# Optimization experiments

Hardware: AMD Instinct MI355X
Metric: run time of the kernel (lower is better)

The kernel has to match this reference:

```python
import jax, jax.numpy as jnp
import numpy as np

N_NODES = 50000
NUM_FEATURES = 64
HIDDEN = 512
NUM_CLASSES = 2
N_EDGES = 800000
BN_EPS = 1e-5


def setup_inputs() -> dict:
    key = jax.random.key(0)
    ks = jax.random.split(key, 10)
    x = jax.random.normal(ks[0], (N_NODES, NUM_FEATURES), dtype=jnp.float32)
    edge_index = jax.random.randint(ks[1], (2, N_EDGES), 0, N_NODES, dtype=jnp.int64)
    # GINConv MLP: Linear(F,H) -> ReLU -> Linear(H,H)
    W1 = jax.random.normal(ks[2], (NUM_FEATURES, HIDDEN), dtype=jnp.float32) * 0.05
    b1 = jnp.zeros((HIDDEN,), dtype=jnp.float32)
    W2 = jax.random.normal(ks[3], (HIDDEN, HIDDEN), dtype=jnp.float32) * 0.05
    b2 = jnp.zeros((HIDDEN,), dtype=jnp.float32)
    # BatchNorm1d(HIDDEN) affine params
    gamma = jnp.ones((HIDDEN,), dtype=jnp.float32)
    beta = jnp.zeros((HIDDEN,), dtype=jnp.float32)
    # classifier: Linear(HIDDEN, NUM_CLASSES)
    Wc = jax.random.normal(ks[4], (HIDDEN, NUM_CLASSES), dtype=jnp.float32) * 0.05
    bc = jnp.zeros((NUM_CLASSES,), dtype=jnp.float32)
    return {"x": x, "edge_index": edge_index, "W1": W1, "b1": b1,
            "W2": W2, "b2": b2, "gamma": gamma, "beta": beta,
            "Wc": Wc, "bc": bc}


def reference(x, edge_index, W1, b1, W2, b2, gamma, beta, Wc, bc):
    # NOTE: the original torch forward returns inside the loop, so exactly ONE
    # GINConv layer runs, followed by batchnorm, relu, dropout(p=0), classifier.
    src, dst = edge_index[0], edge_index[1]
    # GINConv (eps=0): h_i = MLP(x_i + sum_{j -> i} x_j)
    agg = jax.ops.segment_sum(x[src], dst, num_segments=x.shape[0])  # [N, F]
    h = x + agg
    h = jax.nn.relu(h @ W1 + b1) @ W2 + b2  # [N, H]
    # BatchNorm1d in training mode: normalize with batch statistics (biased var)
    mean = jnp.mean(h, axis=0)
    var = jnp.var(h, axis=0)
    h = (h - mean) * jax.lax.rsqrt(var + BN_EPS) * gamma + beta
    h = jax.nn.relu(h)
    # dropout p=0.0 is a no-op
    return h @ Wc + bc  # [N, NUM_CLASSES]
```

## Files before the change

### kernel.cpp

```cpp
#include <hip/hip_runtime.h>
#include <hip/hip_bf16.h>

#define NN 50000
#define MP 50176
#define NF 64
#define NH 512
#define NE 800000
#define NBK 196
#define EBCAP 8192
#define ABLK 391
#define MB 392
#define GRID (MB * 4)
#define CPX (GRID / 8)

typedef __attribute__((ext_vector_type(8))) short bf16x8;
typedef __attribute__((ext_vector_type(4))) float f32x4;

#define GLOAD16(g, l)                                                        \
    __builtin_amdgcn_global_load_lds(                                        \
        (const __attribute__((address_space(1))) unsigned int*)(g),          \
        (__attribute__((address_space(3))) unsigned int*)(l), 16, 0, 0)

__device__ __forceinline__ float bfu(unsigned short u) {
    union { float f; unsigned int i; } c;
    c.i = ((unsigned int)u) << 16;
    return c.f;
}

__global__ void detect_idx(const int* __restrict__ ei, int* __restrict__ flag) {
    if (threadIdx.x == 0 && blockIdx.x == 0) {
        int any = 0;
        for (int i = 0; i < 32; ++i) any |= ei[2 * i + 1];
        *flag = (any == 0) ? 1 : 0;
    }
}

__global__ __launch_bounds__(256) void bucketA(const void* __restrict__ eiv,
                                               const int* __restrict__ flag,
                                               int* __restrict__ bcnt,
                                               int* __restrict__ ebP) {
    __shared__ int hist[NBK];
    __shared__ int lcur[NBK];
    const int tid = threadIdx.x;
    const int chunk = blockIdx.x * 2048;
    const int lim = min(2048, NE - chunk);
    const bool is64 = (*flag != 0);
    const long long* ei64 = (const long long*)eiv;
    const int* ei32 = (const int*)eiv;

    for (int i = tid; i < NBK; i += 256) hist[i] = 0;
    __syncthreads();
    for (int i = tid; i < lim; i += 256) {
        int d = is64 ? (int)ei64[NE + chunk + i] : ei32[NE + chunk + i];
        atomicAdd(&hist[d >> 8], 1);
    }
    __syncthreads();
    for (int i = tid; i < NBK; i += 256) {
        int c = hist[i];
        lcur[i] = c ? atomicAdd(&bcnt[i], c) : 0;
    }
    __syncthreads();
    for (int i = tid; i < lim; i += 256) {
        int s, d;
        if (is64) { s = (int)ei64[chunk + i]; d = (int)ei64[NE + chunk + i]; }
        else      { s = ei32[chunk + i];      d = ei32[NE + chunk + i]; }
        int b = d >> 8;
        int p = atomicAdd(&lcur[b], 1);
        ebP[b * EBCAP + p] = ((d & 255) << 16) | s;
    }
}

__global__ __launch_bounds__(256) void scan_bsum(const int* __restrict__ bsum,
                                                 int* __restrict__ boff) {
    __shared__ int sm[256];
    int tid = threadIdx.x;
    int v = (tid < NBK) ? bsum[tid] : 0;
    sm[tid] = v;
    __syncthreads();
    int acc = v;
#pragma unroll
    for (int off = 1; off < 256; off <<= 1) {
        int t = (tid >= off) ? sm[tid - off] : 0;
        __syncthreads();
        acc += t;
        sm[tid] = acc;
        __syncthreads();
    }
    if (tid < NBK) boff[tid] = acc - v;
}

__global__ __launch_bounds__(256) void bucketB(const int* __restrict__ ebP,
                                               const int* __restrict__ bcnt,
                                               const int* __restrict__ bbase,
                                               int* __restrict__ rowptr,
                                               int* __restrict__ csr) {
    __shared__ int hist[256], sm[256], curs[256];
    const int b = blockIdx.x;
    const int tid = threadIdx.x;
    const int n0 = b << 8;
    const int cnt = bcnt[b];
    const int base = bbase[b];

    hist[tid] = 0;
    __syncthreads();
    for (int i = tid; i < cnt; i += 256)
        atomicAdd(&hist[(ebP[b * EBCAP + i] >> 16) & 255], 1);
    __syncthreads();
    int v = hist[tid];
    sm[tid] = v;
    __syncthreads();
    int acc = v;
#pragma unroll
    for (int off = 1; off < 256; off <<= 1) {
        int t = (tid >= off) ? sm[tid - off] : 0;
        __syncthreads();
        acc += t;
        sm[tid] = acc;
        __syncthreads();
    }
    int excl = acc - v;
    if (n0 + tid < NN) rowptr[n0 + tid] = base + excl;
    curs[tid] = excl;
    __syncthreads();
    for (int i = tid; i < cnt; i += 256) {
        int p = ebP[b * EBCAP + i];
        int lp = atomicAdd(&curs[(p >> 16) & 255], 1);
        csr[base + lp] = p & 0xFFFF;
    }
    if (b == 0 && tid == 0) rowptr[NN] = NE;
}

#define XBLK  (NN * NF / 4 / 256)
#define W1BLK (NF * NH / 256)
#define W2BLK (NH * NH / 256)
__global__ __launch_bounds__(256) void cvt_all(const float* __restrict__ x,
                                               const float* __restrict__ W1,
                                               const float* __restrict__ W2,
                                               __hip_bfloat16* __restrict__ xb,
                                               __hip_bfloat16* __restrict__ w1t,
                                               __hip_bfloat16* __restrict__ w2t) {
    int bb = blockIdx.x;
    if (bb < XBLK) {
        int t = bb * 256 + threadIdx.x;
        float4 v = *(const float4*)&x[t * 4];
        union { ushort4 u; __hip_bfloat16 h[4]; } o;
        o.h[0] = __float2bfloat16(v.x);
        o.h[1] = __float2bfloat16(v.y);
        o.h[2] = __float2bfloat16(v.z);
        o.h[3] = __float2bfloat16(v.w);
        *(ushort4*)&xb[t * 4] = o.u;
    } else if (bb < XBLK + W1BLK) {
        int t = (bb - XBLK) * 256 + threadIdx.x;
        int n = t % NH, k = t / NH;
        w1t[n * NF + k] = __float2bfloat16(W1[t]);
    } else {
        int t = (bb - XBLK - W1BLK) * 256 + threadIdx.x;
        int n = t % NH, k = t / NH;
        w2t[n * NH + k] = __float2bfloat16(W2[t]);
    }
}

__global__ __launch_bounds__(256) void gather(const __hip_bfloat16* __restrict__ xb,
                                              const int* __restrict__ rowptr,
                                              const int* __restrict__ csr,
                                              __hip_bfloat16* __restrict__ h0b) {
    int n = blockIdx.x * 4 + (threadIdx.x >> 6);
    int lane = threadIdx.x & 63;
    int g = lane >> 4;
    int f4 = (lane & 15) * 4;
    if (n >= MP) return;
    if (n >= NN) {
        if (g == 0)
            *(ushort4*)&h0b[(long long)n * NF + f4] = make_ushort4(0, 0, 0, 0);
        return;
    }
    float a0 = 0.f, a1 = 0.f, a2 = 0.f, a3 = 0.f;
    if (g == 0) {
        ushort4 v = *(const ushort4*)&xb[(long long)n * NF + f4];
        a0 = bfu(v.x); a1 = bfu(v.y); a2 = bfu(v.z); a3 = bfu(v.w);
    }
    int e0 = rowptr[n], e1 = rowptr[n + 1];
    for (int e = e0 + g; e < e1; e += 4) {
        int s = csr[e];
        ushort4 v = *(const ushort4*)&xb[(long long)s * NF + f4];
        a0 += bfu(v.x); a1 += bfu(v.y); a2 += bfu(v.z); a3 += bfu(v.w);
    }
    a0 += __shfl_xor(a0, 16); a0 += __shfl_xor(a0, 32);
    a1 += __shfl_xor(a1, 16); a1 += __shfl_xor(a1, 32);
    a2 += __shfl_xor(a2, 16); a2 += __shfl_xor(a2, 32);
    a3 += __shfl_xor(a3, 16); a3 += __shfl_xor(a3, 32);
    if (g == 0) {
        union { ushort4 u; __hip_bfloat16 h[4]; } o;
        o.h[0] = __float2bfloat16(a0);
        o.h[1] = __float2bfloat16(a1);
        o.h[2] = __float2bfloat16(a2);
        o.h[3] = __float2bfloat16(a3);
        *(ushort4*)&h0b[(long long)n * NF + f4] = o.u;
    }
}

__global__ __launch_bounds__(256) void gemm1_staged(const __hip_bfloat16* __restrict__ A,
                                                    const __hip_bfloat16* __restrict__ BT,
                                                    const float* __restrict__ bias,
                                                    __hip_bfloat16* __restrict__ C) {
    __shared__ __hip_bfloat16 As[128 * 64];
    const int orig = blockIdx.x;
    const int L = (orig & 7) * CPX + (orig >> 3);
    const int mb = L >> 2, nb = L & 3;

    const int tid = threadIdx.x;
    const int lane = tid & 63;
    const int w = tid >> 6;
    const int wm = w >> 1, wn = w & 1;
    const long long rbase = (long long)mb * 128;
    const int nbase = nb * 128;
    const int r8  = lane >> 3;
    const int swc = (lane & 7) ^ r8;
    const int key = lane & 7;
    const int lo = lane & 15, hi = lane >> 4;

    {
        const __hip_bfloat16* ga = A + (rbase + w * 32 + r8) * NF + swc * 8;
        __hip_bfloat16* la = As + (w * 32) * 64;
#pragma unroll
        for (int t = 0; t < 4; ++t)
            GLOAD16(ga + t * 8 * NF, la + t * 8 * 64);
    }
    bf16x8 bfr[2][4];
#pragma unroll
    for (int ks = 0; ks < 2; ++ks)
#pragma unroll
        for (int ni = 0; ni < 4; ++ni)
            bfr[ks][ni] = *(const bf16x8*)&BT[(nbase + wn * 64 + ni * 16 + lo) * NF +
                                             ks * 32 + hi * 8];
    __syncthreads();

    f32x4 acc[4][4];
#pragma unroll
    for (int i = 0; i < 4; ++i)
#pragma unroll
        for (int j = 0; j < 4; ++j) acc[i][j] = (f32x4){0.f, 0.f, 0.f, 0.f};

#pragma unroll
    for (int ks = 0; ks < 2; ++ks) {
        bf16x8 af[4];
#pragma unroll
        for (int mi = 0; mi < 4; ++mi)
            af[mi] = *(const bf16x8*)&As[(wm * 64 + mi * 16 + lo) * 64 +
                                         (((ks * 4 + hi) ^ key) * 8)];
#pragma unroll
        for (int mi = 0; mi < 4; ++mi)
#pragma unroll
            for (int ni = 0; ni < 4; ++ni)
                acc[mi][ni] = __builtin_amdgcn_mfma_f32_16x16x32_bf16(
                    af[mi], bfr[ks][ni], acc[mi][ni], 0, 0, 0);
    }

    const int col0 = nbase + wn * 64 + lo;
    const long long row00 = rbase + wm * 64 + hi * 4;
#pragma unroll
    for (int ni = 0; ni < 4; ++ni) {
        int col = col0 + ni * 16;
        float bv = bias[col];
#pragma unroll
        for (int mi = 0; mi < 4; ++mi) {
            long long r0 = row00 + mi * 16;
#pragma unroll
            for (int r = 0; r < 4; ++r) {
                float v = fmaxf(acc[mi][ni][r] + bv, 0.f);
                C[(r0 + r) * NH + col] = __float2bfloat16(v);
            }
        }
    }
}

__global__ __launch_bounds__(256) void gemm2_db(const __hip_bfloat16* __restrict__ A,
                                                const __hip_bfloat16* __restrict__ BT,
                                                const float* __restrict__ bias,
                                                __hip_bfloat16* __restrict__ C,
                                                float* __restrict__ partial) {
    constexpr int BK = 64;
    __shared__ __align__(16) char smem[65536];
    float* smsum = (float*)smem;
    float* smsq  = (float*)(smem + 2048);

    const int orig = blockIdx.x;
    const int L = (orig & 7) * CPX + (orig >> 3);
    const int mb = L >> 2, nb = L & 3;

    const int tid = threadIdx.x;
    const int lane = tid & 63;
    const int w = tid >> 6;
    const int wm = w >> 1, wn = w & 1;
    const long long rbase = (long long)mb * 128;
    const int nbase = nb * 128;
    const int r8  = lane >> 3;
    const int swc = (lane & 7) ^ r8;
    const int key = lane & 7;
    const int lo = lane & 15, hi = lane >> 4;

    const __hip_bfloat16* gaBase =
        A + (rbase + w * 32 + r8) * (long long)NH + swc * 8;
    const __hip_bfloat16* gbBase =
        BT + (long long)(nbase + w * 32 + r8) * NH + swc * 8;
    const int laOff = (w * 32) * BK;

    auto STAGE = [&](int s, int kb) {
        __hip_bfloat16* la = (__hip_bfloat16*)(smem + s * 32768) + laOff;
        __hip_bfloat16* lb = (__hip_bfloat16*)(smem + s * 32768 + 16384) + laOff;
#pragma unroll
        for (int t = 0; t < 4; ++t)
            GLOAD16(gaBase + kb + (long long)t * 8 * NH, la + t * 8 * BK);
#pragma unroll
        for (int t = 0; t < 4; ++t)
            GLOAD16(gbBase + kb + (long long)t * 8 * NH, lb + t * 8 * BK);
    };

    f32x4 acc[4][4];
#pragma unroll
    for (int i = 0; i < 4; ++i)
#pragma unroll
        for (int j = 0; j < 4; ++j) acc[i][j] = (f32x4){0.f, 0.f, 0.f, 0.f};

    STAGE(0, 0);
    STAGE(1, BK);

#pragma unroll
    for (int t = 0; t < 8; ++t) {
        if (t == 7) { asm volatile("s_waitcnt vmcnt(0)" ::: "memory"); }
        else        { asm volatile("s_waitcnt vmcnt(8)" ::: "memory"); }
        __builtin_amdgcn_s_barrier();
        __builtin_amdgcn_sched_barrier(0);

        const __hip_bfloat16* Ac = (const __hip_bfloat16*)(smem + (t & 1) * 32768);
        const __hip_bfloat16* Bc = Ac + 8192;
        __builtin_amdgcn_s_setprio(1);
#pragma unroll
        for (int ks = 0; ks < 2; ++ks) {
            bf16x8 af[4], bfr[4];
#pragma unroll
            for (int mi = 0; mi < 4; ++mi)
                af[mi] = *(const bf16x8*)&Ac[(wm * 64 + mi * 16 + lo) * BK +
                                             (((ks * 4 + hi) ^ key) * 8)];
#pragma unroll
            for (int ni = 0; ni < 4; ++ni)
                bfr[ni] = *(const bf16x8*)&Bc[(wn * 64 + ni * 16 + lo) * BK +
                                              (((ks * 4 + hi) ^ key) * 8)];
#pragma unroll
            for (int mi = 0; mi < 4; ++mi)
#pragma unroll
                for (int ni = 0; ni < 4; ++ni)
                    acc[mi][ni] = __builtin_amdgcn_mfma_f32_16x16x32_bf16(
                        af[mi], bfr[ni], acc[mi][ni], 0, 0, 0);
        }
        __builtin_amdgcn_s_setprio(0);
        __builtin_amdgcn_sched_barrier(0);
        __builtin_amdgcn_s_barrier();
        __builtin_amdgcn_sched_barrier(0);
        if (t < 6) STAGE(t & 1, (t + 2) * BK);
    }

    __syncthreads();
    if (tid < 128) { smsum[tid] = 0.f; smsq[tid] = 0.f; }
    __syncthreads();
    const int col0 = nbase + wn * 64 + lo;
    const long long row00 = rbase + wm * 64 + hi * 4;
#pragma unroll
    for (int ni = 0; ni < 4; ++ni) {
        int col = col0 + ni * 16;
        float bv = bias[col];
        float s = 0.f, q = 0.f;
#pragma unroll
        for (int mi = 0; mi < 4; ++mi) {
            long long r0 = row00 + mi * 16;
#pragma unroll
            for (int r = 0; r < 4; ++r) {
                float v = acc[mi][ni][r] + bv;
                C[(r0 + r) * NH + col] = __float2bfloat16(v);
                if ((r0 + r) < NN) { s += v; q += v * v; }
            }
        }
        s += __shfl_xor(s, 16); s += __shfl_xor(s, 32);
        q += __shfl_xor(q, 16); q += __shfl_xor(q, 32);
        if (lane < 16) {
            atomicAdd(&smsum[wn * 64 + ni * 16 + lane], s);
            atomicAdd(&smsq[wn * 64 + ni * 16 + lane], q);
        }
    }
    __syncthreads();
    if (tid < 128) {
        partial[mb * 1024 + nbase + tid] = smsum[tid];
        partial[mb * 1024 + 512 + nbase + tid] = smsq[tid];
    }
}

__global__ __launch_bounds__(256) void stats_reduce(const float* __restrict__ partial,
                                                    float* __restrict__ stats) {
    int j = blockIdx.x * 256 + threadIdx.x;
    float s = 0.f;
    for (int mb = 0; mb < MB; ++mb) s += partial[mb * 1024 + j];
    stats[j] = s;
}

__global__ __launch_bounds__(256) void bn_cls(const __hip_bfloat16* __restrict__ h2b,
                                              const float* __restrict__ stats,
                                              const float* __restrict__ gamma,
                                              const float* __restrict__ beta,
                                              const float* __restrict__ Wc,
                                              const float* __restrict__ bc,
                                              float* __restrict__ out) {
    int tid = threadIdx.x;
    int lane = tid & 63;
    int k0 = lane * 8;
    float sc[8], sh[8], w0[8], w1[8];
#pragma unroll
    for (int j = 0; j < 8; ++j) {
        int k = k0 + j;
        float mean = stats[k] * (1.0f / NN);
        float var = stats[512 + k] * (1.0f / NN) - mean * mean;
        float rs = rsqrtf(var + 1e-5f);
        float s = gamma[k] * rs;
        sc[j] = s;
        sh[j] = beta[k] - mean * s;
        w0[j] = Wc[2 * k];
        w1[j] = Wc[2 * k + 1];
    }
    float bc0 = bc[0], bc1 = bc[1];
    int wid = blockIdx.x * 4 + (tid >> 6);
    int nw = gridDim.x * 4;
    for (int row = wid; row < NN; row += nw) {
        bf16x8 v8 = *(const bf16x8*)&h2b[(long long)row * NH + k0];
        float a0 = 0.f, a1 = 0.f;
#pragma unroll
        for (int j = 0; j < 8; ++j) {
            float v = __bfloat162float(((const __hip_bfloat16*)&v8)[j]);
            float hn = fmaxf(fmaf(v, sc[j], sh[j]), 0.f);
            a0 = fmaf(hn, w0[j], a0);
            a1 = fmaf(hn, w1[j], a1);
        }
#pragma unroll
        for (int off = 32; off; off >>= 1) {
            a0 += __shfl_xor(a0, off);
            a1 += __shfl_xor(a1, off);
        }
        if (lane == 0) {
            out[(long long)row * 2 + 0] = a0 + bc0;
            out[(long long)row * 2 + 1] = a1 + bc1;
        }
    }
}

extern "C" void kernel_launch(void* const* d_in, const int* in_sizes, int n_in,
                              void* d_out, int out_size, void* d_ws, size_t ws_size,
                              hipStream_t stream) {
    const float* x     = (const float*)d_in[0];
    const void*  ei    = d_in[1];
    const float* W1    = (const float*)d_in[2];
    const float* b1    = (const float*)d_in[3];
    const float* W2    = (const float*)d_in[4];
    const float* b2    = (const float*)d_in[5];
    const float* gamma = (const float*)d_in[6];
    const float* beta  = (const float*)d_in[7];
    const float* Wc    = (const float*)d_in[8];
    const float* bc    = (const float*)d_in[9];
    float* out = (float*)d_out;

    char* base = (char*)d_ws;
    size_t o = 0;
    auto alloc = [&](size_t bytes) {
        char* p = base + o;
        o = (o + bytes + 255) & ~(size_t)255;
        return p;
    };
    __hip_bfloat16* h0b     = (__hip_bfloat16*)alloc((size_t)MP * NF * 2);
    __hip_bfloat16* h1b     = (__hip_bfloat16*)alloc((size_t)MP * NH * 2);
    __hip_bfloat16* h2b     = (__hip_bfloat16*)alloc((size_t)MP * NH * 2);
    __hip_bfloat16* xb      = (__hip_bfloat16*)alloc((size_t)NN * NF * 2);
    __hip_bfloat16* w1t     = (__hip_bfloat16*)alloc((size_t)NH * NF * 2);
    __hip_bfloat16* w2t     = (__hip_bfloat16*)alloc((size_t)NH * NH * 2);
    int*            ebP     = (int*)alloc((size_t)NBK * EBCAP * 4);
    int*            bcnt    = (int*)alloc(256 * 4);
    int*            bbase   = (int*)alloc(256 * 4);
    int*            rowptr  = (int*)alloc((size_t)(NN + 1) * 4);
    int*            csr     = (int*)alloc((size_t)NE * 4);
    float*          partial = (float*)alloc((size_t)MB * 1024 * 4);
    float*          stats   = (float*)alloc(1024 * 4);
    int*            flag    = (int*)alloc(256);

    hipMemsetAsync(bcnt, 0, NBK * 4, stream);
    detect_idx<<<1, 1, 0, stream>>>((const int*)ei, flag);

    bucketA<<<ABLK, 256, 0, stream>>>(ei, flag, bcnt, ebP);
    scan_bsum<<<1, 256, 0, stream>>>(bcnt, bbase);
    bucketB<<<NBK, 256, 0, stream>>>(ebP, bcnt, bbase, rowptr, csr);

    cvt_all<<<XBLK + W1BLK + W2BLK, 256, 0, stream>>>(x, W1, W2, xb, w1t, w2t);
    gather<<<MP / 4, 256, 0, stream>>>(xb, rowptr, csr, h0b);

    gemm1_staged<<<GRID, 256, 0, stream>>>(h0b, w1t, b1, h1b);
    gemm2_db<<<GRID, 256, 0, stream>>>(h1b, w2t, b2, h2b, partial);

    stats_reduce<<<4, 256, 0, stream>>>(partial, stats);
    bn_cls<<<512, 256, 0, stream>>>(h2b, stats, gamma, beta, Wc, bc, out);
}
```

Baseline: 165.9 us.

## Keep full weight panel resident in LDS and loop blocks over M-tiles in gemm2

Replaces the 128x128-tile second GEMM with a persistent-style kernel. Each 512-thread block loads an entire 128-column by 512-deep W2 panel into LDS once, then streams seven 128-row A tiles through a double buffer. This aims to stop re-fetching B for every output tile and to cut the block count. BN partial statistics are now written per warp-row without an LDS atomic reduction, which doubles the partial buffer and the stats_reduce loop length. The 160KB LDS footprint allows only one block per CU, and 224 blocks leave some CUs idle.

```diff
diff --git a/kernel.cpp b/kernel.cpp
--- a/kernel.cpp
+++ b/kernel.cpp
@@ -12,6 +12,9 @@
 #define MB 392
 #define GRID (MB * 4)
 #define CPX (GRID / 8)
+#define G2BLK 224
+#define CPX2 (G2BLK / 8)
+#define MTPB 7
 
 typedef __attribute__((ext_vector_type(8))) short bf16x8;
 typedef __attribute__((ext_vector_type(4))) float f32x4;
@@ -274,123 +277,128 @@
     }
 }
 
-__global__ __launch_bounds__(256) void gemm2_db(const __hip_bfloat16* __restrict__ A,
-                                                const __hip_bfloat16* __restrict__ BT,
-                                                const float* __restrict__ bias,
-                                                __hip_bfloat16* __restrict__ C,
-                                                float* __restrict__ partial) {
+__global__ __launch_bounds__(512) void gemm2_panel(const __hip_bfloat16* __restrict__ A,
+                                                   const __hip_bfloat16* __restrict__ BT,
+                                                   const float* __restrict__ bias,
+                                                   __hip_bfloat16* __restrict__ C,
+                                                   float* __restrict__ partial) {
     constexpr int BK = 64;
-    __shared__ __align__(16) char smem[65536];
-    float* smsum = (float*)smem;
-    float* smsq  = (float*)(smem + 2048);
+    __shared__ __align__(16) char smem[163840];
+    __hip_bfloat16* Bp = (__hip_bfloat16*)smem;
+    __hip_bfloat16* Ab0 = (__hip_bfloat16*)(smem + 131072);
+    __hip_bfloat16* Ab1 = (__hip_bfloat16*)(smem + 147456);
 
     const int orig = blockIdx.x;
-    const int L = (orig & 7) * CPX + (orig >> 3);
-    const int mb = L >> 2, nb = L & 3;
+    const int L = (orig & 7) * CPX2 + (orig >> 3);
+    const int stripe = L / 56;
+    const int q = L % 56;
+    const int nbase = stripe * 128;
 
     const int tid = threadIdx.x;
     const int lane = tid & 63;
     const int w = tid >> 6;
-    const int wm = w >> 1, wn = w & 1;
-    const long long rbase = (long long)mb * 128;
-    const int nbase = nb * 128;
-    const int r8  = lane >> 3;
+    const int wm = w >> 2, wn = w & 3;
+    const int r8 = lane >> 3;
     const int swc = (lane & 7) ^ r8;
-    const int key = lane & 7;
     const int lo = lane & 15, hi = lane >> 4;
 
-    const __hip_bfloat16* gaBase =
-        A + (rbase + w * 32 + r8) * (long long)NH + swc * 8;
-    const __hip_bfloat16* gbBase =
-        BT + (long long)(nbase + w * 32 + r8) * NH + swc * 8;
-    const int laOff = (w * 32) * BK;
-
-    auto STAGE = [&](int s, int kb) {
-        __hip_bfloat16* la = (__hip_bfloat16*)(smem + s * 32768) + laOff;
-        __hip_bfloat16* lb = (__hip_bfloat16*)(smem + s * 32768 + 16384) + laOff;
-#pragma unroll
-        for (int t = 0; t < 4; ++t)
-            GLOAD16(gaBase + kb + (long long)t * 8 * NH, la + t * 8 * BK);
-#pragma unroll
-        for (int t = 0; t < 4; ++t)
-            GLOAD16(gbBase + kb + (long long)t * 8 * NH, lb + t * 8 * BK);
-    };
-
-    f32x4 acc[4][4];
-#pragma unroll
-    for (int i = 0; i < 4; ++i)
-#pragma unroll
-        for (int j = 0; j < 4; ++j) acc[i][j] = (f32x4){0.f, 0.f, 0.f, 0.f};
-
-    STAGE(0, 0);
-    STAGE(1, BK);
-
-#pragma unroll
-    for (int t = 0; t < 8; ++t) {
-        if (t == 7) { asm volatile("s_waitcnt vmcnt(0)" ::: "memory"); }
-        else        { asm volatile("s_waitcnt vmcnt(8)" ::: "memory"); }
-        __builtin_amdgcn_s_barrier();
-        __builtin_amdgcn_sched_barrier(0);
-
-        const __hip_bfloat16* Ac = (const __hip_bfloat16*)(smem + (t & 1) * 32768);
-        const __hip_bfloat16* Bc = Ac + 8192;
-        __builtin_amdgcn_s_setprio(1);
-#pragma unroll
-        for (int ks = 0; ks < 2; ++ks) {
-            bf16x8 af[4], bfr[4];
-#pragma unroll
-            for (int mi = 0; mi < 4; ++mi)
-                af[mi] = *(const bf16x8*)&Ac[(wm * 64 + mi * 16 + lo) * BK +
-                                             (((ks * 4 + hi) ^ key) * 8)];
-#pragma unroll
-            for (int ni = 0; ni < 4; ++ni)
-                bfr[ni] = *(const bf16x8*)&Bc[(wn * 64 + ni * 16 + lo) * BK +
-                                              (((ks * 4 + hi) ^ key) * 8)];
-#pragma unroll
-            for (int mi = 0; mi < 4; ++mi)
-#pragma unroll
-                for (int ni = 0; ni < 4; ++ni)
-                    acc[mi][ni] = __builtin_amdgcn_mfma_f32_16x16x32_bf16(
-                        af[mi], bfr[ni], acc[mi][ni], 0, 0, 0);
-        }
-        __builtin_amdgcn_s_setprio(0);
-        __builtin_amdgcn_sched_barrier(0);
-        __builtin_amdgcn_s_barrier();
-        __builtin_amdgcn_sched_barrier(0);
-        if (t < 6) STAGE(t & 1, (t + 2) * BK);
-    }
-
-    __syncthreads();
-    if (tid < 128) { smsum[tid] = 0.f; smsq[tid] = 0.f; }
-    __syncthreads();
-    const int col0 = nbase + wn * 64 + lo;
-    const long long row00 = rbase + wm * 64 + hi * 4;
-#pragma unroll
-    for (int ni = 0; ni < 4; ++ni) {
-        int col = col0 + ni * 16;
-        float bv = bias[col];
-        float s = 0.f, q = 0.f;
-#pragma unroll
-        for (int mi = 0; mi < 4; ++mi) {
-            long long r0 = row00 + mi * 16;
-#pragma unroll
-            for (int r = 0; r < 4; ++r) {
-                float v = acc[mi][ni][r] + bv;
-                C[(r0 + r) * NH + col] = __float2bfloat16(v);
-                if ((r0 + r) < NN) { s += v; q += v * v; }
+    {
+        const int colbase = w * 16;
+#pragma unroll
+        for (int c = 0; c < 16; ++c) {
+            int col = colbase + c;
+            int gch = (lane & ~7) | ((lane & 7) ^ (col & 7));
+            GLOAD16(BT + (long long)(nbase + col) * NH + gch * 8,
+                    Bp + col * 512 + lane * 8);
+        }
+    }
+    __syncthreads();
+
+    for (int mt = 0; mt < MTPB; ++mt) {
+        const int mb = q * MTPB + mt;
+        const long long rbase = (long long)mb * 128;
+        const __hip_bfloat16* gaBase =
+            A + (rbase + w * 16 + r8) * (long long)NH + swc * 8;
+        __hip_bfloat16* laBase0 = Ab0 + (w * 16) * BK;
+        __hip_bfloat16* laBase1 = Ab1 + (w * 16) * BK;
+
+        auto STAGE = [&](int s, int kb) {
+            __hip_bfloat16* la = s ? laBase1 : laBase0;
+#pragma unroll
+            for (int t = 0; t < 2; ++t)
+                GLOAD16(gaBase + kb + (long long)t * 8 * NH, la + t * 8 * BK);
+        };
+
+        f32x4 acc[4][2];
+#pragma unroll
+        for (int i = 0; i < 4; ++i)
+#pragma unroll
+            for (int j = 0; j < 2; ++j) acc[i][j] = (f32x4){0.f, 0.f, 0.f, 0.f};
+
+        STAGE(0, 0);
+        STAGE(1, BK);
+
+#pragma unroll
+        for (int t = 0; t < 8; ++t) {
+            if (t == 7) { asm volatile("s_waitcnt vmcnt(0)" ::: "memory"); }
+            else        { asm volatile("s_waitcnt vmcnt(2)" ::: "memory"); }
+            __builtin_amdgcn_s_barrier();
+            __builtin_amdgcn_sched_barrier(0);
+
+            const __hip_bfloat16* Ac = (t & 1) ? Ab1 : Ab0;
+#pragma unroll
+            for (int ks = 0; ks < 2; ++ks) {
+                bf16x8 af[4], bfr[2];
+#pragma unroll
+                for (int mi = 0; mi < 4; ++mi) {
+                    int row = wm * 64 + mi * 16 + lo;
+                    af[mi] = *(const bf16x8*)&Ac[row * BK +
+                                                 (((ks * 4 + hi) ^ (row & 7)) * 8)];
+                }
+#pragma unroll
+                for (int ni = 0; ni < 2; ++ni) {
+                    int col = wn * 32 + ni * 16 + lo;
+                    bfr[ni] = *(const bf16x8*)&Bp[col * 512 + t * 64 +
+                                                  (((ks * 4 + hi) ^ (col & 7)) * 8)];
+                }
+#pragma unroll
+                for (int mi = 0; mi < 4; ++mi)
+#pragma unroll
+                    for (int ni = 0; ni < 2; ++ni)
+                        acc[mi][ni] = __builtin_amdgcn_mfma_f32_16x16x32_bf16(
+                            af[mi], bfr[ni], acc[mi][ni], 0, 0, 0);
             }
-        }
-        s += __shfl_xor(s, 16); s += __shfl_xor(s, 32);
-        q += __shfl_xor(q, 16); q += __shfl_xor(q, 32);
-        if (lane < 16) {
-            atomicAdd(&smsum[wn * 64 + ni * 16 + lane], s);
-            atomicAdd(&smsq[wn * 64 + ni * 16 + lane], q);
-        }
-    }
-    __syncthreads();
-    if (tid < 128) {
-        partial[mb * 1024 + nbase + tid] = smsum[tid];
-        partial[mb * 1024 + 512 + nbase + tid] = smsq[tid];
+            __builtin_amdgcn_sched_barrier(0);
+            __builtin_amdgcn_s_barrier();
+            __builtin_amdgcn_sched_barrier(0);
+            if (t < 6) STAGE(t & 1, (t + 2) * BK);
+        }
+
+        const int col0 = nbase + wn * 32 + lo;
+        const long long row00 = rbase + wm * 64 + hi * 4;
+#pragma unroll
+        for (int ni = 0; ni < 2; ++ni) {
+            int col = col0 + ni * 16;
+            float bv = bias[col];
+            float s = 0.f, qq = 0.f;
+#pragma unroll
+            for (int mi = 0; mi < 4; ++mi) {
+                long long r0 = row00 + mi * 16;
+#pragma unroll
+                for (int r = 0; r < 4; ++r) {
+                    float v = acc[mi][ni][r] + bv;
+                    C[(r0 + r) * NH + col] = __float2bfloat16(v);
+                    if ((r0 + r) < NN) { s += v; qq += v * v; }
+                }
+            }
+            s  += __shfl_xor(s, 16);  s += __shfl_xor(s, 32);
+            qq += __shfl_xor(qq, 16); qq += __shfl_xor(qq, 32);
+            if (lane < 16) {
+                int cc = nbase + wn * 32 + ni * 16 + lane;
+                partial[(mb * 2 + wm) * 1024 + cc] = s;
+                partial[(mb * 2 + wm) * 1024 + 512 + cc] = qq;
+            }
+        }
     }
 }
 
@@ -398,7 +406,7 @@
                                                     float* __restrict__ stats) {
     int j = blockIdx.x * 256 + threadIdx.x;
     float s = 0.f;
-    for (int mb = 0; mb < MB; ++mb) s += partial[mb * 1024 + j];
+    for (int sl = 0; sl < MB * 2; ++sl) s += partial[sl * 1024 + j];
     stats[j] = s;
 }
 
@@ -483,7 +491,7 @@
     int*            bbase   = (int*)alloc(256 * 4);
     int*            rowptr  = (int*)alloc((size_t)(NN + 1) * 4);
     int*            csr     = (int*)alloc((size_t)NE * 4);
-    float*          partial = (float*)alloc((size_t)MB * 1024 * 4);
+    float*          partial = (float*)alloc((size_t)MB * 2 * 1024 * 4);
     float*          stats   = (float*)alloc(1024 * 4);
     int*            flag    = (int*)alloc(256);
 
@@ -498,7 +506,7 @@
     gather<<<MP / 4, 256, 0, stream>>>(xb, rowptr, csr, h0b);
 
     gemm1_staged<<<GRID, 256, 0, stream>>>(h0b, w1t, b1, h1b);
-    gemm2_db<<<GRID, 256, 0, stream>>>(h1b, w2t, b2, h2b, partial);
+    gemm2_panel<<<G2BLK, 512, 0, stream>>>(h1b, w2t, b2, h2b, partial);
 
     stats_reduce<<<4, 256, 0, stream>>>(partial, stats);
     bn_cls<<<512, 256, 0, stream>>>(h2b, stats, gamma, beta, Wc, bc, out);
```

Result: slower. 185.7 us (+11.9%).
